# Kernel optimization log

Hardware: AMD Instinct MI355X
Metric: run time of the kernel (lower is better)

Reference implementation:

```python
import jax, jax.numpy as jnp
import numpy as np
import math

NHEAD = 16
FACTOR = 5


def setup_inputs() -> dict:
    key = jax.random.key(0)
    ks = jax.random.split(key, 10)
    B, L, Dm = 2, 2048, 1024
    x = jax.random.normal(ks[0], (B, L, Dm), dtype=jnp.float32)
    w = lambda k: jax.random.normal(k, (Dm, Dm), dtype=jnp.float32) * 0.02
    b = lambda k: jax.random.normal(k, (Dm,), dtype=jnp.float32) * 0.02
    return {
        "x": x,
        "Wq": w(ks[1]), "bq": b(ks[2]),
        "Wk": w(ks[3]), "bk": b(ks[4]),
        "Wv": w(ks[5]), "bv": b(ks[6]),
        "Wo": w(ks[7]), "bo": b(ks[8]),
    }


def reference(x, Wq, bq, Wk, bk, Wv, bv, Wo, bo):
    B, L, Dm = x.shape
    H = NHEAD
    D = Dm // H
    # U = number of top scores kept per query row (ProbSparse sparsity level)
    U = min(L, int(FACTOR * math.log(L)) if L > 1 else L)

    def proj(W, b):
        # torch Linear: x @ W^T + b ; then [B,L,H,D] -> [B,H,L,D]
        return (x @ W.T + b).reshape(B, L, H, D).transpose(0, 2, 1, 3)

    Q = proj(Wq, bq)
    K = proj(Wk, bk)
    V = proj(Wv, bv)

    scores = jnp.einsum("bhqd,bhkd->bhqk", Q, K) / math.sqrt(D)  # [B,H,L,L]
    # kth-largest score per row; keep entries >= threshold (ties kept, matching torch semantics)
    thresh = jax.lax.top_k(scores, U)[0][..., -1:]  # [B,H,L,1]
    scores = jnp.where(scores < thresh, -jnp.inf, scores)
    attn = jax.nn.softmax(scores, axis=-1)  # dropout is identity in eval
    context = jnp.einsum("bhqk,bhkd->bhqd", attn, V)
    context = context.transpose(0, 2, 1, 3).reshape(B, L, Dm)
    return context @ Wo.T + bo
```

## Files before the change

kernel.cpp:

```cpp
#include <hip/hip_runtime.h>
#include <math.h>

#define BB 2
#define LL 2048
#define DM 1024
#define NH 16
#define HD 64

__device__ __forceinline__ unsigned mono32(float f) {
    unsigned u = __float_as_uint(f);
    return (u & 0x80000000u) ? ~u : (u | 0x80000000u);
}
__device__ __forceinline__ float unmono32(unsigned m) {
    const unsigned u = (m & 0x80000000u) ? (m & 0x7FFFFFFFu) : ~m;
    return __uint_as_float(u);
}

__global__ __launch_bounds__(256) void transpose1024(
    const float* __restrict__ in, float* __restrict__ out)
{
    __shared__ float t[32][33];
    const int bx = blockIdx.x * 32, by = blockIdx.y * 32;
    const int tx = threadIdx.x & 31, ty = threadIdx.x >> 5;
    for (int r = ty; r < 32; r += 8)
        t[r][tx] = in[(size_t)(by + r) * DM + bx + tx];
    __syncthreads();
    for (int r = ty; r < 32; r += 8)
        out[(size_t)(bx + r) * DM + by + tx] = t[tx][r];
}

__global__ __launch_bounds__(256) void proj_emul(
    const float* __restrict__ x, const float* __restrict__ Wt,
    const float* __restrict__ bias, float* __restrict__ outp)
{
    __shared__ float xs[8][DM];
    const int tid = threadIdx.x;
    const int n4  = tid * 4;
    const int m0  = blockIdx.x * 8;

    for (int i = tid; i < 8 * 256; i += 256) {
        const int r = i >> 8, c4 = (i & 255) << 2;
        *(float4*)&xs[r][c4] = *(const float4*)&x[(size_t)(m0 + r) * DM + c4];
    }
    __syncthreads();

    const int kbound[4] = {0, 384, 704, 1024};
    float S[8][4] = {};
#pragma unroll
    for (int p = 0; p < 3; p++) {
        float P[8][4] = {};
        for (int k = kbound[p]; k < kbound[p + 1]; k += 4) {
            const float4 w0 = *(const float4*)&Wt[(size_t)(k + 0) * DM + n4];
            const float4 w1 = *(const float4*)&Wt[(size_t)(k + 1) * DM + n4];
            const float4 w2 = *(const float4*)&Wt[(size_t)(k + 2) * DM + n4];
            const float4 w3 = *(const float4*)&Wt[(size_t)(k + 3) * DM + n4];
#pragma unroll
            for (int m = 0; m < 8; m++) {
                const float4 xv = *(const float4*)&xs[m][k];
                P[m][0] = fmaf(xv.x, w0.x, P[m][0]);
                P[m][1] = fmaf(xv.x, w0.y, P[m][1]);
                P[m][2] = fmaf(xv.x, w0.z, P[m][2]);
                P[m][3] = fmaf(xv.x, w0.w, P[m][3]);
                P[m][0] = fmaf(xv.y, w1.x, P[m][0]);
                P[m][1] = fmaf(xv.y, w1.y, P[m][1]);
                P[m][2] = fmaf(xv.y, w1.z, P[m][2]);
                P[m][3] = fmaf(xv.y, w1.w, P[m][3]);
                P[m][0] = fmaf(xv.z, w2.x, P[m][0]);
                P[m][1] = fmaf(xv.z, w2.y, P[m][1]);
                P[m][2] = fmaf(xv.z, w2.z, P[m][2]);
                P[m][3] = fmaf(xv.z, w2.w, P[m][3]);
                P[m][0] = fmaf(xv.w, w3.x, P[m][0]);
                P[m][1] = fmaf(xv.w, w3.y, P[m][1]);
                P[m][2] = fmaf(xv.w, w3.z, P[m][2]);
                P[m][3] = fmaf(xv.w, w3.w, P[m][3]);
            }
        }
#pragma unroll
        for (int m = 0; m < 8; m++) {
#pragma unroll
            for (int j = 0; j < 4; j++) S[m][j] += P[m][j];
        }
    }

    const float4 b4v = *(const float4*)&bias[n4];
    const int h = n4 / HD, d0 = n4 % HD;
#pragma unroll
    for (int m = 0; m < 8; m++) {
        const int mm = m0 + m;
        const int b = mm / LL, l = mm % LL;
        float4 o;
        o.x = S[m][0] + b4v.x; o.y = S[m][1] + b4v.y;
        o.z = S[m][2] + b4v.z; o.w = S[m][3] + b4v.w;
        *(float4*)&outp[(((size_t)b * NH + h) * LL + l) * HD + d0] = o;
    }
}

template <int MODE>
__global__ __launch_bounds__(256) void gemm_f32(
    const float* __restrict__ A, const float* __restrict__ W,
    const float* __restrict__ bias, float* __restrict__ out,
    int M, int N, int K)
{
    __shared__ float As[16][64];
    __shared__ float Bs[16][64];
    const int tid = threadIdx.x;
    const int m0 = blockIdx.y * 64;
    const int n0 = blockIdx.x * 64;
    const int tx = tid & 15, ty = tid >> 4;
    const int lr = tid >> 2, lc = (tid & 3) * 4;

    float acc[4][4] = {};

    for (int k0 = 0; k0 < K; k0 += 16) {
        float4 a4 = *(const float4*)&A[(size_t)(m0 + lr) * K + k0 + lc];
        float4 b4 = *(const float4*)&W[(size_t)(n0 + lr) * K + k0 + lc];
        __syncthreads();
        As[lc + 0][lr] = a4.x; As[lc + 1][lr] = a4.y;
        As[lc + 2][lr] = a4.z; As[lc + 3][lr] = a4.w;
        Bs[lc + 0][lr] = b4.x; Bs[lc + 1][lr] = b4.y;
        Bs[lc + 2][lr] = b4.z; Bs[lc + 3][lr] = b4.w;
        __syncthreads();
#pragma unroll
        for (int kk = 0; kk < 16; kk++) {
            float4 av = *(const float4*)&As[kk][ty * 4];
            float4 bv = *(const float4*)&Bs[kk][tx * 4];
            float a[4] = {av.x, av.y, av.z, av.w};
            float b[4] = {bv.x, bv.y, bv.z, bv.w};
#pragma unroll
            for (int i = 0; i < 4; i++)
#pragma unroll
                for (int j = 0; j < 4; j++)
                    acc[i][j] = fmaf(a[i], b[j], acc[i][j]);
        }
    }

#pragma unroll
    for (int i = 0; i < 4; i++) {
        const int m = m0 + ty * 4 + i;
#pragma unroll
        for (int j = 0; j < 4; j++) {
            const int n = n0 + tx * 4 + j;
            const float v = acc[i][j] + bias[n];
            if (MODE == 0) {
                const int b = m / LL, l = m % LL;
                const int h = n / HD, d = n % HD;
                out[(((size_t)b * NH + h) * LL + l) * HD + d] = v;
            } else {
                out[(size_t)m * N + n] = v;
            }
        }
    }
}

__global__ __launch_bounds__(256) void score_np(
    const float* __restrict__ Qf, const float* __restrict__ Kf,
    unsigned* __restrict__ scw, int bh0)
{
#pragma clang fp contract(off)
    const int tid  = threadIdx.x;
    const int lane = tid & 63;
    const int wv   = tid >> 6;
    const int l0   = blockIdx.x * 16;
    const int bhl  = blockIdx.y;
    const int bh   = bh0 + bhl;

    __shared__ float kt[2][64][68];
    __shared__ float qsh[16][64];

    const float* __restrict__ Kb = Kf + (size_t)bh * LL * HD;

    {
        const int r = tid >> 4, d4q = tid & 15;
        *(float4*)&qsh[r][d4q * 4] =
            *(const float4*)&Qf[((size_t)bh * LL + l0 + r) * HD + d4q * 4];
    }
#pragma unroll
    for (int i = 0; i < 4; i++) {
        const int idx = i * 256 + tid;
        *(float4*)&kt[0][idx >> 4][(idx & 15) * 4] =
            *(const float4*)&Kb[(size_t)(idx >> 4) * HD + (idx & 15) * 4];
    }
    __syncthreads();

    const int r0 = wv * 4;
    unsigned* __restrict__ s0 = scw + ((size_t)bhl * LL + l0 + r0 + 0) * LL;
    unsigned* __restrict__ s1 = scw + ((size_t)bhl * LL + l0 + r0 + 1) * LL;
    unsigned* __restrict__ s2 = scw + ((size_t)bhl * LL + l0 + r0 + 2) * LL;
    unsigned* __restrict__ s3 = scw + ((size_t)bhl * LL + l0 + r0 + 3) * LL;

    for (int tile = 0; tile < 32; tile++) {
        const int buf = tile & 1;
        float4 pf0, pf1, pf2, pf3;
        if (tile < 31) {
            const float* src = Kb + (size_t)(tile + 1) * 64 * HD;
            pf0 = *(const float4*)&src[(size_t)((0 * 256 + tid) >> 4) * HD + ((0 * 256 + tid) & 15) * 4];
            pf1 = *(const float4*)&src[(size_t)((1 * 256 + tid) >> 4) * HD + ((1 * 256 + tid) & 15) * 4];
            pf2 = *(const float4*)&src[(size_t)((2 * 256 + tid) >> 4) * HD + ((2 * 256 + tid) & 15) * 4];
            pf3 = *(const float4*)&src[(size_t)((3 * 256 + tid) >> 4) * HD + ((3 * 256 + tid) & 15) * 4];
        }

        float ax0 = 0, ay0 = 0, az0 = 0, aw0 = 0;
        float ax1 = 0, ay1 = 0, az1 = 0, aw1 = 0;
        float ax2 = 0, ay2 = 0, az2 = 0, aw2 = 0;
        float ax3 = 0, ay3 = 0, az3 = 0, aw3 = 0;
        const float* krow = &kt[buf][lane][0];
        const float* q0 = &qsh[r0 + 0][0];
        const float* q1 = &qsh[r0 + 1][0];
        const float* q2 = &qsh[r0 + 2][0];
        const float* q3 = &qsh[r0 + 3][0];
#pragma unroll
        for (int t = 0; t < 4; t++) {
#pragma unroll
            for (int sub = 3; sub >= 0; sub--) {
                const int d4 = 4 * t + sub;
                const float4 kf = *(const float4*)&krow[d4 * 4];
                const float4 qa = *(const float4*)&q0[d4 * 4];
                const float4 qb = *(const float4*)&q1[d4 * 4];
                const float4 qc = *(const float4*)&q2[d4 * 4];
                const float4 qd = *(const float4*)&q3[d4 * 4];
                ax0 = qa.x * kf.x + ax0; ay0 = qa.y * kf.y + ay0;
                az0 = qa.z * kf.z + az0; aw0 = qa.w * kf.w + aw0;
                ax1 = qb.x * kf.x + ax1; ay1 = qb.y * kf.y + ay1;
                az1 = qb.z * kf.z + az1; aw1 = qb.w * kf.w + aw1;
                ax2 = qc.x * kf.x + ax2; ay2 = qc.y * kf.y + ay2;
                az2 = qc.z * kf.z + az2; aw2 = qc.w * kf.w + aw2;
                ax3 = qd.x * kf.x + ax3; ay3 = qd.y * kf.y + ay3;
                az3 = qd.z * kf.z + az3; aw3 = qd.w * kf.w + aw3;
            }
        }
        s0[tile * 64 + lane] = mono32(((ax0 + ay0) + (az0 + aw0)) * 0.125f);
        s1[tile * 64 + lane] = mono32(((ax1 + ay1) + (az1 + aw1)) * 0.125f);
        s2[tile * 64 + lane] = mono32(((ax2 + ay2) + (az2 + aw2)) * 0.125f);
        s3[tile * 64 + lane] = mono32(((ax3 + ay3) + (az3 + aw3)) * 0.125f);

        if (tile < 31) {
            *(float4*)&kt[buf ^ 1][(0 * 256 + tid) >> 4][((0 * 256 + tid) & 15) * 4] = pf0;
            *(float4*)&kt[buf ^ 1][(1 * 256 + tid) >> 4][((1 * 256 + tid) & 15) * 4] = pf1;
            *(float4*)&kt[buf ^ 1][(2 * 256 + tid) >> 4][((2 * 256 + tid) & 15) * 4] = pf2;
            *(float4*)&kt[buf ^ 1][(3 * 256 + tid) >> 4][((3 * 256 + tid) & 15) * 4] = pf3;
            __syncthreads();
        }
    }
}

__global__ __launch_bounds__(256) void select_np(
    const unsigned* __restrict__ scw, const float* __restrict__ Vf,
    float* __restrict__ ctx, int U, int bh0)
{
#pragma clang fp contract(off)
    const int tid  = threadIdx.x;
    const int lane = tid & 63;
    const int wv   = tid >> 6;
    const int l0   = blockIdx.x * 8;
    const int bhl  = blockIdx.y;
    const int bh   = bh0 + bhl;
    const int b    = bh / NH;
    const int h    = bh % NH;

    __shared__ float wls[8][64];
    __shared__ int   kls[8][64];

    const unsigned long long laneLT = (1ull << lane) - 1ull;
    const float* __restrict__ Vb = Vf + (size_t)bh * LL * HD;

#pragma unroll
    for (int rr8 = 0; rr8 < 2; rr8++) {
        const int rr = wv * 2 + rr8;
        const unsigned* __restrict__ srow =
            scw + ((size_t)bhl * LL + l0 + rr) * LL;

        unsigned mv[32];
#pragma unroll
        for (int j = 0; j < 32; j++) mv[j] = srow[lane + 64 * j];

        unsigned lo = 0u, hi = 0xFFFFFFFFu;
        while (lo < hi) {
            const unsigned span = hi - lo;
            const unsigned mid = lo + (span >> 1) + (span & 1u);
            int c = 0;
#pragma unroll
            for (int j = 0; j < 32; j++)
                c += (int)__popcll(__ballot(mv[j] >= mid));
            if (c >= U) lo = mid; else hi = mid - 1u;
        }

        unsigned mk = 0;
#pragma unroll
        for (int j = 0; j < 32; j++)
            if (mv[j] >= lo) mk = (mv[j] > mk) ? mv[j] : mk;
#pragma unroll
        for (int off = 32; off > 0; off >>= 1) {
            const unsigned o = __shfl_xor(mk, off, 64);
            mk = (o > mk) ? o : mk;
        }
        const float mx = unmono32(mk);

        int n = 0;
#pragma unroll
        for (int j = 0; j < 32; j++) {
            const bool p = (mv[j] >= lo);
            const unsigned long long ball = __ballot(p);
            if (p) {
                const int pos = n + (int)__popcll(ball & laneLT);
                if (pos < 64) {
                    kls[rr][pos] = lane + 64 * j;
                    wls[rr][pos] = expf(unmono32(mv[j]) - mx);
                }
            }
            n += (int)__popcll(ball);
        }
        if (n > 64) n = 64;

        float dl = (lane < n) ? wls[rr][lane] : 0.0f;
#pragma unroll
        for (int off = 32; off > 0; off >>= 1) dl += __shfl_xor(dl, off, 64);
        const float rden = 1.0f / dl;

        float acc = 0.0f;
        for (int c = 0; c < n; c++)
            acc = fmaf(wls[rr][c], Vb[(size_t)kls[rr][c] * HD + lane], acc);

        ctx[((size_t)b * LL + l0 + rr) * DM + h * HD + lane] = acc * rden;
    }
}

extern "C" void kernel_launch(void* const* d_in, const int* in_sizes, int n_in,
                              void* d_out, int out_size, void* d_ws, size_t ws_size,
                              hipStream_t stream)
{
    const float* x  = (const float*)d_in[0];
    const float* Wq = (const float*)d_in[1];
    const float* bq = (const float*)d_in[2];
    const float* Wk = (const float*)d_in[3];
    const float* bk = (const float*)d_in[4];
    const float* Wv = (const float*)d_in[5];
    const float* bv = (const float*)d_in[6];
    const float* Wo = (const float*)d_in[7];
    const float* bo = (const float*)d_in[8];
    float* out = (float*)d_out;

    const size_t E = (size_t)BB * NH * LL * HD;
    float* Wt1 = (float*)d_ws;
    float* Wt2 = Wt1 + (size_t)DM * DM;
    float* Qf  = Wt2 + (size_t)DM * DM;
    float* Kf  = Qf + E;
    float* Vf  = Kf + E;
    float* ctx = Vf + E;
    unsigned* scw = (unsigned*)(ctx + E);

    int U = (int)(5.0 * log((double)LL));
    if (U > LL) U = LL;

    const size_t base_bytes = (size_t)72 * 1024 * 1024;
    const size_t per_bh = (size_t)LL * LL * 4;
    size_t avail = (ws_size > base_bytes) ? (ws_size - base_bytes) : 0;
    int chunk = (int)(avail / per_bh);
    if (chunk < 1) chunk = 1;
    if (chunk > 8) chunk = 8;

    const int M = BB * LL;
    dim3 blk(256);
    dim3 gT(DM / 32, DM / 32);
    dim3 gP(M / 8);
    dim3 g64(DM / 64, M / 64);

    hipLaunchKernelGGL(transpose1024, gT, blk, 0, stream, Wq, Wt1);
    hipLaunchKernelGGL(transpose1024, gT, blk, 0, stream, Wk, Wt2);
    hipLaunchKernelGGL(proj_emul, gP, blk, 0, stream, x, Wt1, bq, Qf);
    hipLaunchKernelGGL(proj_emul, gP, blk, 0, stream, x, Wt2, bk, Kf);
    hipLaunchKernelGGL((gemm_f32<0>), g64, blk, 0, stream, x, Wv, bv, Vf, M, DM, DM);

    for (int bh0 = 0; bh0 < BB * NH; bh0 += chunk) {
        int nb = BB * NH - bh0;
        if (nb > chunk) nb = chunk;
        dim3 gA(LL / 16, nb);
        dim3 gS(LL / 8, nb);
        hipLaunchKernelGGL(score_np,  gA, blk, 0, stream, Qf, Kf, scw, bh0);
        hipLaunchKernelGGL(select_np, gS, blk, 0, stream, scw, Vf, ctx, U, bh0);
    }

    hipLaunchKernelGGL((gemm_f32<1>), g64, blk, 0, stream, ctx, Wo, bo, out, M, DM, DM);
}
```

Measured before the change: 1.681 ms.

## Tile score kernel over 256-key chunks with 4x4 register blocking

Replaces the double-buffered 64-key K tile loop in score_np with a single-buffered 256-key tile loaded per iteration, so each thread computes 4 queries x 4 keys per step. Each K and Q register value is reused across four accumulators, which cuts LDS reads per FMA and reduces the number of barriers from 32 to 16. In exchange it drops the prefetch/compute overlap, raises LDS use to about 70KB per block, and holds 64 float accumulators, which may lower occupancy. Each thread's global K load is a whole 256-byte row, so the loads are strided across the wavefront.

```diff
diff --git a/kernel.cpp b/kernel.cpp
--- a/kernel.cpp
+++ b/kernel.cpp
@@ -45,6 +45,7 @@
     __syncthreads();
 
     const int kbound[4] = {0, 384, 704, 1024};
+
     float S[8][4] = {};
 #pragma unroll
     for (int p = 0; p < 3; p++) {
@@ -164,7 +165,7 @@
     const int bhl  = blockIdx.y;
     const int bh   = bh0 + bhl;
 
-    __shared__ float kt[2][64][68];
+    __shared__ float kt[256][68];
     __shared__ float qsh[16][64];
 
     const float* __restrict__ Kb = Kf + (size_t)bh * LL * HD;
@@ -174,13 +175,6 @@
         *(float4*)&qsh[r][d4q * 4] =
             *(const float4*)&Qf[((size_t)bh * LL + l0 + r) * HD + d4q * 4];
     }
-#pragma unroll
-    for (int i = 0; i < 4; i++) {
-        const int idx = i * 256 + tid;
-        *(float4*)&kt[0][idx >> 4][(idx & 15) * 4] =
-            *(const float4*)&Kb[(size_t)(idx >> 4) * HD + (idx & 15) * 4];
-    }
-    __syncthreads();
 
     const int r0 = wv * 4;
     unsigned* __restrict__ s0 = scw + ((size_t)bhl * LL + l0 + r0 + 0) * LL;
@@ -188,57 +182,64 @@
     unsigned* __restrict__ s2 = scw + ((size_t)bhl * LL + l0 + r0 + 2) * LL;
     unsigned* __restrict__ s3 = scw + ((size_t)bhl * LL + l0 + r0 + 3) * LL;
 
-    for (int tile = 0; tile < 32; tile++) {
-        const int buf = tile & 1;
-        float4 pf0, pf1, pf2, pf3;
-        if (tile < 31) {
-            const float* src = Kb + (size_t)(tile + 1) * 64 * HD;
-            pf0 = *(const float4*)&src[(size_t)((0 * 256 + tid) >> 4) * HD + ((0 * 256 + tid) & 15) * 4];
-            pf1 = *(const float4*)&src[(size_t)((1 * 256 + tid) >> 4) * HD + ((1 * 256 + tid) & 15) * 4];
-            pf2 = *(const float4*)&src[(size_t)((2 * 256 + tid) >> 4) * HD + ((2 * 256 + tid) & 15) * 4];
-            pf3 = *(const float4*)&src[(size_t)((3 * 256 + tid) >> 4) * HD + ((3 * 256 + tid) & 15) * 4];
-        }
-
-        float ax0 = 0, ay0 = 0, az0 = 0, aw0 = 0;
-        float ax1 = 0, ay1 = 0, az1 = 0, aw1 = 0;
-        float ax2 = 0, ay2 = 0, az2 = 0, aw2 = 0;
-        float ax3 = 0, ay3 = 0, az3 = 0, aw3 = 0;
-        const float* krow = &kt[buf][lane][0];
-        const float* q0 = &qsh[r0 + 0][0];
-        const float* q1 = &qsh[r0 + 1][0];
-        const float* q2 = &qsh[r0 + 2][0];
-        const float* q3 = &qsh[r0 + 3][0];
+    for (int kp = 0; kp < 8; kp++) {
+        __syncthreads();
+        {
+            const float* src = Kb + ((size_t)kp * 256 + tid) * HD;
+#pragma unroll
+            for (int i = 0; i < 16; i++)
+                *(float4*)&kt[tid][i * 4] = *(const float4*)&src[i * 4];
+        }
+        __syncthreads();
+
+        float4 acc[4][4];
+#pragma unroll
+        for (int r = 0; r < 4; r++)
+#pragma unroll
+            for (int j = 0; j < 4; j++)
+                acc[r][j] = make_float4(0.f, 0.f, 0.f, 0.f);
+
 #pragma unroll
         for (int t = 0; t < 4; t++) {
 #pragma unroll
             for (int sub = 3; sub >= 0; sub--) {
                 const int d4 = 4 * t + sub;
-                const float4 kf = *(const float4*)&krow[d4 * 4];
-                const float4 qa = *(const float4*)&q0[d4 * 4];
-                const float4 qb = *(const float4*)&q1[d4 * 4];
-                const float4 qc = *(const float4*)&q2[d4 * 4];
-                const float4 qd = *(const float4*)&q3[d4 * 4];
-                ax0 = qa.x * kf.x + ax0; ay0 = qa.y * kf.y + ay0;
-                az0 = qa.z * kf.z + az0; aw0 = qa.w * kf.w + aw0;
-                ax1 = qb.x * kf.x + ax1; ay1 = qb.y * kf.y + ay1;
-                az1 = qb.z * kf.z + az1; aw1 = qb.w * kf.w + aw1;
-                ax2 = qc.x * kf.x + ax2; ay2 = qc.y * kf.y + ay2;
-                az2 = qc.z * kf.z + az2; aw2 = qc.w * kf.w + aw2;
-                ax3 = qd.x * kf.x + ax3; ay3 = qd.y * kf.y + ay3;
-                az3 = qd.z * kf.z + az3; aw3 = qd.w * kf.w + aw3;
+                float4 kf0 = *(const float4*)&kt[0 * 64 + lane][d4 * 4];
+                float4 kf1 = *(const float4*)&kt[1 * 64 + lane][d4 * 4];
+                float4 kf2 = *(const float4*)&kt[2 * 64 + lane][d4 * 4];
+                float4 kf3 = *(const float4*)&kt[3 * 64 + lane][d4 * 4];
+                float4 qv0 = *(const float4*)&qsh[r0 + 0][d4 * 4];
+                float4 qv1 = *(const float4*)&qsh[r0 + 1][d4 * 4];
+                float4 qv2 = *(const float4*)&qsh[r0 + 2][d4 * 4];
+                float4 qv3 = *(const float4*)&qsh[r0 + 3][d4 * 4];
+#pragma unroll
+                for (int r = 0; r < 4; r++) {
+                    const float4 q = (r == 0) ? qv0 : (r == 1) ? qv1
+                                   : (r == 2) ? qv2 : qv3;
+#pragma unroll
+                    for (int j = 0; j < 4; j++) {
+                        const float4 k = (j == 0) ? kf0 : (j == 1) ? kf1
+                                       : (j == 2) ? kf2 : kf3;
+                        acc[r][j].x = q.x * k.x + acc[r][j].x;
+                        acc[r][j].y = q.y * k.y + acc[r][j].y;
+                        acc[r][j].z = q.z * k.z + acc[r][j].z;
+                        acc[r][j].w = q.w * k.w + acc[r][j].w;
+                    }
+                }
             }
         }
-        s0[tile * 64 + lane] = mono32(((ax0 + ay0) + (az0 + aw0)) * 0.125f);
-        s1[tile * 64 + lane] = mono32(((ax1 + ay1) + (az1 + aw1)) * 0.125f);
-        s2[tile * 64 + lane] = mono32(((ax2 + ay2) + (az2 + aw2)) * 0.125f);
-        s3[tile * 64 + lane] = mono32(((ax3 + ay3) + (az3 + aw3)) * 0.125f);
-
-        if (tile < 31) {
-            *(float4*)&kt[buf ^ 1][(0 * 256 + tid) >> 4][((0 * 256 + tid) & 15) * 4] = pf0;
-            *(float4*)&kt[buf ^ 1][(1 * 256 + tid) >> 4][((1 * 256 + tid) & 15) * 4] = pf1;
-            *(float4*)&kt[buf ^ 1][(2 * 256 + tid) >> 4][((2 * 256 + tid) & 15) * 4] = pf2;
-            *(float4*)&kt[buf ^ 1][(3 * 256 + tid) >> 4][((3 * 256 + tid) & 15) * 4] = pf3;
-            __syncthreads();
+
+#pragma unroll
+        for (int j = 0; j < 4; j++) {
+            const int kk = kp * 256 + j * 64 + lane;
+            s0[kk] = mono32(((acc[0][j].x + acc[0][j].y) +
+                             (acc[0][j].z + acc[0][j].w)) * 0.125f);
+            s1[kk] = mono32(((acc[1][j].x + acc[1][j].y) +
+                             (acc[1][j].z + acc[1][j].w)) * 0.125f);
+            s2[kk] = mono32(((acc[2][j].x + acc[2][j].y) +
+                             (acc[2][j].z + acc[2][j].w)) * 0.125f);
+            s3[kk] = mono32(((acc[3][j].x + acc[3][j].y) +
+                             (acc[3][j].z + acc[3][j].w)) * 0.125f);
         }
     }
 }
```

Result: slower. 1.995 ms (+18.7%).
